# Optimization experiments

Measured on AMD Instinct MI355X. Metric: run time of the kernel, lower is better.

## Reference

```python
import jax, jax.numpy as jnp
import numpy as np

BS, F, C, H, W = 2, 8, 64, 128, 128
HEADS = 4

def build_edges(bs, f):
    rows, cols, ec = [], [], 0
    for b in range(bs):
        s = b * (2 * f + 2)
        v = list(range(s, s + f)); d = list(range(s + f, s + 2 * f))
        t = s + 2 * f; g = t + 1
        for grp in (v, d, v + d, v + d, v + d + [t], [t], [g]):
            rows += grp; cols += [ec] * len(grp); ec += 1
    return np.asarray(rows, np.int32), np.asarray(cols, np.int32), ec

ROW, COL, NUM_EDGES = build_edges(BS, F)

def conv2d_s2(x, w, b):  # Conv2d k3 s2 p1 + ReLU
    y = jax.lax.conv_general_dilated(x, w, (2, 2), [(1, 1), (1, 1)],
        dimension_numbers=('NCHW', 'OIHW', 'NCHW'))
    return jax.nn.relu(y + b[None, :, None, None])

def conv_t2(x, w, b):  # ConvTranspose2d k3 s2 p1 op1 + ReLU; w: (in,out,3,3)
    wt = jnp.flip(w, (2, 3)).transpose(1, 0, 2, 3)
    y = jax.lax.conv_general_dilated(x, wt, (1, 1), [(1, 2), (1, 2)],
        lhs_dilation=(2, 2), dimension_numbers=('NCHW', 'OIHW', 'NCHW'))
    return jax.nn.relu(y + b[None, :, None, None])

def layer_norm(x, eps=1e-5):  # affine params are default ones/zeros
    mu = x.mean(-1, keepdims=True)
    var = ((x - mu) ** 2).mean(-1, keepdims=True)
    return (x - mu) / jnp.sqrt(var + eps)

def group_norm(x, groups=32, eps=1e-5):
    n, c = x.shape
    xg = x.reshape(n, groups, c // groups)
    mu = xg.mean(-1, keepdims=True)
    var = ((xg - mu) ** 2).mean(-1, keepdims=True)
    return ((xg - mu) / jnp.sqrt(var + eps)).reshape(n, c)

def se_layer(x, w1, w2):  # squeeze over node dim 0
    y = jax.nn.sigmoid(jax.nn.relu(x.mean(0) @ w1.T) @ w2.T)
    return x * y

def hypergraph_conv(x, lin_w, att, edge_w, edge_attr, out_ch):
    # PyG HypergraphConv, use_attention=True, attention_mode='node', heads=4,
    # concat=False, bias=False, eval mode (dropout inactive)
    n = x.shape[0]
    xl = (x @ lin_w.T).reshape(n, HEADS, out_ch)
    ea = (edge_attr @ lin_w.T).reshape(-1, HEADS, out_ch)
    a = (jnp.concatenate([xl[ROW], ea[COL]], axis=-1) * att).sum(-1)  # (E, heads)
    a = jax.nn.leaky_relu(a, 0.2)
    a = jnp.exp(a - jax.ops.segment_max(a, COL, num_segments=NUM_EDGES)[COL])
    a = a / (jax.ops.segment_sum(a, COL, num_segments=NUM_EDGES)[COL] + 1e-16)
    D = jax.ops.segment_sum(edge_w[COL], ROW, num_segments=n)
    D = jnp.where(D > 0, 1.0 / D, 0.0)
    B = jax.ops.segment_sum(jnp.ones(ROW.shape[0], x.dtype), COL, num_segments=NUM_EDGES)
    B = jnp.where(B > 0, 1.0 / B, 0.0)
    e = jax.ops.segment_sum(B[COL][:, None, None] * a[:, :, None] * xl[ROW], COL, num_segments=NUM_EDGES)
    o = jax.ops.segment_sum(D[ROW][:, None, None] * a[:, :, None] * e[COL], ROW, num_segments=n)
    return o.mean(1)  # concat=False -> head mean

def setup_inputs() -> dict:
    key = jax.random.key(0)
    ks = jax.random.split(key, 32)
    def n(k, shape, s=1.0):
        return jax.random.normal(k, shape, jnp.float32) * s
    def u(k, shape):
        return jax.random.uniform(k, shape, jnp.float32)
    return {
        'vision_feat': n(ks[0], (BS, F, C, H, W)), 'vision_pos': n(ks[1], (BS, F, C, H, W), 0.1),
        'motion_feat': n(ks[2], (BS, F, C, H, W)), 'motion_pos': n(ks[3], (BS, F, C, H, W), 0.1),
        'text_feat': n(ks[4], (BS, C, 16)), 'text_pos': n(ks[5], (BS, C, 16), 0.1),
        'cv1_w': n(ks[6], (2 * C, C, 3, 3), 0.04), 'cv1_b': n(ks[7], (2 * C,), 0.01),
        'cv2_w': n(ks[8], (4 * C, 2 * C, 3, 3), 0.03), 'cv2_b': n(ks[9], (4 * C,), 0.01),
        'dc1_w': n(ks[10], (2 * C, C, 3, 3), 0.04), 'dc1_b': n(ks[11], (2 * C,), 0.01),
        'dc2_w': n(ks[12], (4 * C, 2 * C, 3, 3), 0.03), 'dc2_b': n(ks[13], (4 * C,), 0.01),
        'tc1_w': n(ks[14], (4 * C, 2 * C, 3, 3), 0.03), 'tc1_b': n(ks[15], (2 * C,), 0.01),
        'tc2_w': n(ks[16], (2 * C, C, 3, 3), 0.04), 'tc2_b': n(ks[17], (C,), 0.01),
        'lin1_w': n(ks[18], (HEADS * 8 * C, 4 * C), 0.06), 'att1': n(ks[19], (1, HEADS, 16 * C), 0.05),
        'lin2_w': n(ks[20], (HEADS * 4 * C, 8 * C), 0.04), 'att2': n(ks[21], (1, HEADS, 8 * C), 0.05),
        'ew1': u(ks[22], (2 * F * BS + 2,)), 'ew2': u(ks[23], (2 * F * BS + 2,)),
        'ea1': u(ks[24], (2 * F * BS + 2, 4 * C)), 'ea2': u(ks[25], (2 * F * BS + 2, 8 * C)),
        'se1_w1': n(ks[26], (8 * C // 16, 8 * C), 0.06), 'se1_w2': n(ks[27], (8 * C, 8 * C // 16), 0.15),
        'se2_w1': n(ks[28], (4 * C // 16, 4 * C), 0.08), 'se2_w2': n(ks[29], (4 * C, 4 * C // 16), 0.2),
    }

def reference(vision_feat, vision_pos, motion_feat, motion_pos, text_feat, text_pos,
              cv1_w, cv1_b, cv2_w, cv2_b, dc1_w, dc1_b, dc2_w, dc2_b,
              tc1_w, tc1_b, tc2_w, tc2_b, lin1_w, att1, lin2_w, att2,
              ew1, ew2, ea1, ea2, se1_w1, se1_w2, se2_w1, se2_w2):
    bs, f, c, h, w = vision_feat.shape
    # text_pool: AdaptiveMaxPool1d(4) on L=16 -> exact windows of 4; view(bs,-1)
    tn = (text_feat + text_pos).reshape(bs, c, 4, 4).max(-1).reshape(bs, 4 * c)
    v0 = (vision_feat + vision_pos).reshape(bs * f, c, h, w)
    v1 = conv2d_s2(v0, cv1_w, cv1_b)          # (bs*f, 2c, h/2, w/2)
    v2 = conv2d_s2(v1, cv2_w, cv2_b)          # (bs*f, 4c, h/4, w/4)
    vn = layer_norm(v2.max((2, 3)))           # AdaptiveMaxPool2d(1) + LayerNorm
    d0 = (motion_feat + motion_pos).reshape(bs * f, c, h, w)
    dn = layer_norm(conv2d_s2(conv2d_s2(d0, dc1_w, dc1_b), dc2_w, dc2_b).max((2, 3)))
    vb = vn.reshape(bs, f, 4 * c); db = dn.reshape(bs, f, 4 * c)
    obs = tn + (vb + db).mean(1)              # observer = mean(text+v+d) over frames
    x = jnp.concatenate([vb, db, tn[:, None], obs[:, None]], axis=1).reshape(bs * (2 * f + 2), 4 * c)
    x = se_layer(group_norm(jax.nn.relu(hypergraph_conv(x, lin1_w, att1, ew1, ea1, 8 * c))), se1_w1, se1_w2)
    x = se_layer(group_norm(jax.nn.relu(hypergraph_conv(x, lin2_w, att2, ew2, ea2, 4 * c))), se2_w1, se2_w2)
    xb = x.reshape(bs, 2 * f + 2, 4 * c)
    # obs_pool: AdaptiveMaxPool1d(c) on L=4c -> windows of 4
    observers = (tn + xb[:, -1]).reshape(bs, c, 4).max(-1)
    vg = xb[:, :f].reshape(bs * f, 4 * c)
    # bilinear upsample of 1x1 == broadcast; transconv doubles size so the
    # subsequent F.interpolate calls to (h/2,w/2) and (h,w) are identities
    vr = v2 + vg[:, :, None, None]
    vr = v1 + conv_t2(vr, tc1_w, tc1_b)
    vr = v0 + conv_t2(vr, tc2_w, tc2_b)
    return vr, observers
```

## Files before the change

### kernel.cpp

```cpp
#include <hip/hip_runtime.h>
#include <hip/hip_bf16.h>
#include <cstddef>
#include <cstdint>

#define DEV_INLINE __device__ __forceinline__

typedef __attribute__((ext_vector_type(8))) short short8;
typedef __attribute__((ext_vector_type(4))) float f32x4;
typedef __attribute__((ext_vector_type(2))) float f32x2;
typedef __attribute__((ext_vector_type(4))) unsigned short us4;

DEV_INLINE unsigned short f2bf(float f) {
  uint32_t u = __builtin_bit_cast(uint32_t, f);
  uint32_t r = (u + 0x7fffu + ((u >> 16) & 1u)) >> 16;
  return (unsigned short)r;
}
DEV_INLINE float bf2f(unsigned short u) {
  return __builtin_bit_cast(float, (uint32_t)u << 16);
}

__device__ __constant__ int c_cs[15] = {0,8,16,32,48,65,66,67,75,83,99,115,132,133,134};
__device__ __constant__ int c_row[134] = {
  0,1,2,3,4,5,6,7,
  8,9,10,11,12,13,14,15,
  0,1,2,3,4,5,6,7,8,9,10,11,12,13,14,15,
  0,1,2,3,4,5,6,7,8,9,10,11,12,13,14,15,
  0,1,2,3,4,5,6,7,8,9,10,11,12,13,14,15,16,
  16,
  17,
  18,19,20,21,22,23,24,25,
  26,27,28,29,30,31,32,33,
  18,19,20,21,22,23,24,25,26,27,28,29,30,31,32,33,
  18,19,20,21,22,23,24,25,26,27,28,29,30,31,32,33,
  18,19,20,21,22,23,24,25,26,27,28,29,30,31,32,33,34,
  34,
  35
};
__device__ __constant__ int c_col[134] = {
  0,0,0,0,0,0,0,0,
  1,1,1,1,1,1,1,1,
  2,2,2,2,2,2,2,2,2,2,2,2,2,2,2,2,
  3,3,3,3,3,3,3,3,3,3,3,3,3,3,3,3,
  4,4,4,4,4,4,4,4,4,4,4,4,4,4,4,4,4,
  5,
  6,
  7,7,7,7,7,7,7,7,
  8,8,8,8,8,8,8,8,
  9,9,9,9,9,9,9,9,9,9,9,9,9,9,9,9,
  10,10,10,10,10,10,10,10,10,10,10,10,10,10,10,10,
  11,11,11,11,11,11,11,11,11,11,11,11,11,11,11,11,11,
  12,
  13
};

__global__ __launch_bounds__(256) void k_prep(const float* __restrict__ a,
                                              const float* __restrict__ b,
                                              unsigned short* __restrict__ o) {
  int bid = blockIdx.x;
  int xb = bid & 1, y = (bid >> 1) & 127, n = bid >> 8;
  __shared__ unsigned int su[32][65];
  int t = threadIdx.x;
  const size_t base = ((size_t)n * 64) * 16384 + (size_t)y * 128 + xb * 64;
  float4 A0[2], B0[2], A1[2], B1[2];
#pragma unroll
  for (int it = 0; it < 2; ++it) {
    int i = t + it * 256;
    int cpair = i >> 4, x4 = i & 15;
    size_t off = base + (size_t)(2 * cpair) * 16384 + x4 * 4;
    A0[it] = *reinterpret_cast<const float4*>(a + off);
    B0[it] = *reinterpret_cast<const float4*>(b + off);
    A1[it] = *reinterpret_cast<const float4*>(a + off + 16384);
    B1[it] = *reinterpret_cast<const float4*>(b + off + 16384);
  }
#pragma unroll
  for (int it = 0; it < 2; ++it) {
    int i = t + it * 256;
    int cpair = i >> 4, x4 = i & 15;
    unsigned int* row = &su[cpair][x4 * 4];
    row[0] = (unsigned int)f2bf(A0[it].x + B0[it].x) | ((unsigned int)f2bf(A1[it].x + B1[it].x) << 16);
    row[1] = (unsigned int)f2bf(A0[it].y + B0[it].y) | ((unsigned int)f2bf(A1[it].y + B1[it].y) << 16);
    row[2] = (unsigned int)f2bf(A0[it].z + B0[it].z) | ((unsigned int)f2bf(A1[it].z + B1[it].z) << 16);
    row[3] = (unsigned int)f2bf(A0[it].w + B0[it].w) | ((unsigned int)f2bf(A1[it].w + B1[it].w) << 16);
  }
  __syncthreads();
  unsigned int* op = (unsigned int*)(o + (((size_t)n * 128 + y) * 128 + xb * 64) * 64);
#pragma unroll
  for (int it = 0; it < 2; ++it) {
    int i = t + it * 256;
    int x = i >> 3, cq = i & 7;
    uint4 v;
    v.x = su[cq * 4 + 0][x];
    v.y = su[cq * 4 + 1][x];
    v.z = su[cq * 4 + 2][x];
    v.w = su[cq * 4 + 3][x];
    *reinterpret_cast<uint4*>(op + x * 32 + cq * 4) = v;
  }
}

__global__ void k_wtrans_all(const float* __restrict__ cv1w, const float* __restrict__ dc1w,
                             const float* __restrict__ cv2w, const float* __restrict__ dc2w,
                             const float* __restrict__ tc1w, const float* __restrict__ tc2w,
                             unsigned short* __restrict__ wtb) {
  int idx = blockIdx.x * 256 + threadIdx.x;
  const float* src; int off, lci, lco; bool tra;
  if (idx < 73728)        { src = cv1w; off = 0;       lci = 6; lco = 7; tra = false; }
  else if (idx < 147456)  { src = dc1w; off = 73728;   lci = 6; lco = 7; tra = false; }
  else if (idx < 442368)  { src = cv2w; off = 147456;  lci = 7; lco = 8; tra = false; }
  else if (idx < 737280)  { src = dc2w; off = 442368;  lci = 7; lco = 8; tra = false; }
  else if (idx < 1032192) { src = tc1w; off = 737280;  lci = 8; lco = 7; tra = true;  }
  else if (idx < 1105920) { src = tc2w; off = 1032192; lci = 7; lco = 6; tra = true;  }
  else return;
  int l = idx - off;
  int ci = l & ((1 << lci) - 1);
  int r = l >> lci;
  int co = r & ((1 << lco) - 1);
  int tap = r >> lco;
  size_t si = tra ? (((size_t)ci << lco) + co) * 9 + tap
                  : (((size_t)co << lci) + ci) * 9 + tap;
  wtb[idx] = f2bf(src[si]);
}

template<int CI, int CO, int HO, int WO, int ROUT>
__global__ __launch_bounds__(512, 3) void k_conv_mfma(
    const unsigned short* __restrict__ in,
    const unsigned short* __restrict__ wT,
    const float* __restrict__ bias,
    unsigned short* __restrict__ outn) {
  constexpr int HIN = HO * 2, WIN = WO * 2;
  constexpr int XHP = WO + 2;
  constexpr int R = 2 * ROUT + 1;
  constexpr int NPOS = R * 2 * XHP;
  constexpr int NCH = NPOS * 4;
  constexpr int NCS = CI / 32;
  constexpr int KIT = (NCH + 511) / 512;
  constexpr int CB = CO / 128;
  constexpr int OB = HO / ROUT;
  __shared__ short8 sIn[NPOS * 5];
  int bid = blockIdx.x;
  int cb = bid % CB; bid /= CB;
  int oyb = bid % OB; int n = bid / OB;
  int tid = threadIdx.x;
  int wid = tid >> 6, lane = tid & 63;
  int wm = wid >> 1, wn = wid & 1;
  int llo = lane & 15, lhi = lane >> 4;
  f32x4 acc[2][2] = {};
  const int iy0 = oyb * (2 * ROUT) - 1;
  short8 rv[KIT];
  auto loadr = [&](int cs) {
#pragma unroll
    for (int k = 0; k < KIT; ++k) {
      int i = tid + k * 512;
      short8 v = {};
      if (i < NCH) {
        int c = i & 3, q = i >> 2;
        int xh = q % XHP; int q2 = q / XHP;
        int p = q2 & 1, l = q2 >> 1;
        int x = 2 * xh + p - 1;
        int iy = iy0 + l;
        if (x >= 0 && x < WIN && iy >= 0 && iy < HIN)
          v = *reinterpret_cast<const short8*>(in + ((((size_t)n * HIN + iy) * WIN + x) * CI + cs * 32 + c * 8));
      }
      rv[k] = v;
    }
  };
  auto writes = [&]() {
#pragma unroll
    for (int k = 0; k < KIT; ++k) {
      int i = tid + k * 512;
      if (i < NCH) sIn[(i >> 2) * 5 + (i & 3)] = rv[k];
    }
  };
  loadr(0);
  for (int cs = 0; cs < NCS; ++cs) {
    writes();
    __syncthreads();
    if (cs + 1 < NCS) loadr(cs + 1);
    short8 afr9[9][2];
#pragma unroll
    for (int tap = 0; tap < 9; ++tap)
#pragma unroll
      for (int m = 0; m < 2; ++m) {
        int co = cb * 128 + wm * 32 + m * 16 + llo;
        afr9[tap][m] = *reinterpret_cast<const short8*>(wT + (((size_t)tap * CO + co) * CI + cs * 32 + lhi * 8));
      }
#pragma unroll
    for (int tap = 0; tap < 9; ++tap) {
      const int ky = tap / 3, kx = tap % 3;
      short8 bfr[2];
#pragma unroll
      for (int n2 = 0; n2 < 2; ++n2) {
        int pix = wn * 32 + n2 * 16 + llo;
        int oyl = (ROUT == 2) ? (pix >> 5) : 0;
        int ox = pix - oyl * WO;
        int lrow = 2 * oyl + ky;
        int pos = (lrow * 2 + (kx & 1)) * XHP + ox + (kx >> 1);
        bfr[n2] = sIn[pos * 5 + lhi];
      }
#pragma unroll
      for (int m = 0; m < 2; ++m)
#pragma unroll
        for (int n2 = 0; n2 < 2; ++n2)
          acc[m][n2] = __builtin_amdgcn_mfma_f32_16x16x32_bf16(afr9[tap][m], bfr[n2], acc[m][n2], 0, 0, 0);
    }
    __syncthreads();
  }
#pragma unroll
  for (int m = 0; m < 2; ++m) {
    int co0 = cb * 128 + wm * 32 + m * 16 + lhi * 4;
    f32x4 bv = *reinterpret_cast<const f32x4*>(bias + co0);
#pragma unroll
    for (int n2 = 0; n2 < 2; ++n2) {
      int pix = wn * 32 + n2 * 16 + llo;
      int oyl = (ROUT == 2) ? (pix >> 5) : 0;
      int ox = pix - oyl * WO;
      int oy = oyb * ROUT + oyl;
      us4 pk;
      pk[0] = f2bf(fmaxf(acc[m][n2][0] + bv[0], 0.f));
      pk[1] = f2bf(fmaxf(acc[m][n2][1] + bv[1], 0.f));
      pk[2] = f2bf(fmaxf(acc[m][n2][2] + bv[2], 0.f));
      pk[3] = f2bf(fmaxf(acc[m][n2][3] + bv[3], 0.f));
      *reinterpret_cast<us4*>(outn + ((((size_t)n * HO + oy) * WO + ox) * CO + co0)) = pk;
    }
  }
}

template<int CI, int CO, int Hi, int Wi, int QR, bool OBF, bool GADD>
__global__ __launch_bounds__(256, 3) void k_deconv_mfma(
    const unsigned short* __restrict__ in,
    const unsigned short* __restrict__ wT,
    const float* __restrict__ bias,
    const unsigned short* __restrict__ resn,
    const float* __restrict__ gsrc,
    unsigned short* __restrict__ outn,
    float* __restrict__ outc) {
  constexpr int QC = 64 / QR;
  constexpr int WP = Wi + 1;
  constexpr int NPOS = (QR + 1) * WP;
  constexpr int NCH = NPOS * 4;
  constexpr int NCS = CI / 32;
  constexpr int KIT = (NCH + 255) / 256;
  constexpr int CB = CO / 64;
  constexpr int OB = Hi / QR;
  constexpr int Ho = Hi * 2, Wo = Wi * 2;
  __shared__ short8 sIn[NPOS * 5];
  int bid = blockIdx.x;
  int cb = bid % CB; bid /= CB;
  int oyb = bid % OB; int n = bid / OB;
  int tid = threadIdx.x;
  int wid = tid >> 6, lane = tid & 63;
  int wm = wid >> 1, wn = wid & 1;
  int llo = lane & 15, lhi = lane >> 4;
  int qy0 = oyb * QR;
  const float* g = nullptr;
  if constexpr (GADD) g = gsrc + ((size_t)((n >> 3) * 18 + (n & 7))) * 256;
  f32x4 acc[4][2][2] = {};
  constexpr int tap_p[9] = {3,2,3,1,0,1,3,2,3};
  constexpr int tap_b[9] = {3,2,2,1,0,0,1,0,0};
  short8 rv[KIT];
  auto loadr = [&](int cs) {
#pragma unroll
    for (int k = 0; k < KIT; ++k) {
      int i = tid + k * 256;
      short8 v = {};
      if (i < NCH) {
        int c = i & 3, q = i >> 2;
        int x = q % WP, l = q / WP;
        int iy = qy0 + l;
        if (x < Wi && iy < Hi) {
          v = *reinterpret_cast<const short8*>(in + (((size_t)(n * Hi + iy) * Wi + x) * CI + cs * 32 + c * 8));
          if constexpr (GADD) {
#pragma unroll
            for (int j = 0; j < 8; ++j) {
              float fv = bf2f((unsigned short)v[j]) + g[cs * 32 + c * 8 + j];
              v[j] = (short)f2bf(fv);
            }
          }
        }
      }
      rv[k] = v;
    }
  };
  auto writes = [&]() {
#pragma unroll
    for (int k = 0; k < KIT; ++k) {
      int i = tid + k * 256;
      if (i < NCH) sIn[(i >> 2) * 5 + (i & 3)] = rv[k];
    }
  };
  loadr(0);
  for (int cs = 0; cs < NCS; ++cs) {
    writes();
    __syncthreads();
    if (cs + 1 < NCS) loadr(cs + 1);
    short8 bfr[2][4];
#pragma unroll
    for (int n2 = 0; n2 < 2; ++n2) {
      int pix = wn * 32 + n2 * 16 + llo;
      int qyl = pix / QC, qx = pix % QC;
#pragma unroll
      for (int bs = 0; bs < 4; ++bs) {
        int pos = (qyl + (bs >> 1)) * WP + qx + (bs & 1);
        bfr[n2][bs] = sIn[pos * 5 + lhi];
      }
    }
#pragma unroll
    for (int m = 0; m < 2; ++m) {
      short8 afr9[9];
#pragma unroll
      for (int tap = 0; tap < 9; ++tap) {
        int co = cb * 64 + wm * 32 + m * 16 + llo;
        afr9[tap] = *reinterpret_cast<const short8*>(wT + (((size_t)tap * CO + co) * CI + cs * 32 + lhi * 8));
      }
#pragma unroll
      for (int tap = 0; tap < 9; ++tap)
#pragma unroll
        for (int n2 = 0; n2 < 2; ++n2)
          acc[tap_p[tap]][m][n2] = __builtin_amdgcn_mfma_f32_16x16x32_bf16(
              afr9[tap], bfr[n2][tap_b[tap]], acc[tap_p[tap]][m][n2], 0, 0, 0);
    }
    __syncthreads();
  }
#pragma unroll
  for (int m = 0; m < 2; ++m) {
    int co0 = cb * 64 + wm * 32 + m * 16 + lhi * 4;
    f32x4 bv = *reinterpret_cast<const f32x4*>(bias + co0);
#pragma unroll
    for (int n2 = 0; n2 < 2; ++n2) {
      int pix = wn * 32 + n2 * 16 + llo;
      int qyl = pix / QC, qx = pix % QC;
      int qy = qy0 + qyl;
      if constexpr (OBF) {
#pragma unroll
        for (int p = 0; p < 4; ++p) {
          int oy = 2 * qy + (p >> 1);
          int ox = 2 * qx + (p & 1);
          size_t ad = ((size_t)(n * Ho + oy) * Wo + ox) * CO + co0;
          us4 r = *reinterpret_cast<const us4*>(resn + ad);
          us4 pk;
#pragma unroll
          for (int c = 0; c < 4; ++c)
            pk[c] = f2bf(bf2f(r[c]) + fmaxf(acc[p][m][n2][c] + bv[c], 0.f));
          *reinterpret_cast<us4*>(outn + ad) = pk;
        }
      } else {
        int qx2 = 2 * qx;
#pragma unroll
        for (int dy = 0; dy < 2; ++dy) {
          int oy = 2 * qy + dy;
          size_t rb = ((size_t)(n * Ho + oy) * Wo + qx2) * CO + co0;
          us4 r0 = *reinterpret_cast<const us4*>(resn + rb);
          us4 r1 = *reinterpret_cast<const us4*>(resn + rb + CO);
#pragma unroll
          for (int c = 0; c < 4; ++c) {
            f32x2 st;
            st[0] = bf2f(r0[c]) + fmaxf(acc[dy * 2][m][n2][c] + bv[c], 0.f);
            st[1] = bf2f(r1[c]) + fmaxf(acc[dy * 2 + 1][m][n2][c] + bv[c], 0.f);
            __builtin_nontemporal_store(st,
                reinterpret_cast<f32x2*>(outc + ((size_t)(n * CO + co0 + c) * Ho + oy) * Wo + qx2));
          }
        }
      }
    }
  }
}

__global__ __launch_bounds__(256) void k_max_part(const unsigned short* __restrict__ x,
                                                  float* __restrict__ pmax) {
  int n = blockIdx.x >> 3, pg = blockIdx.x & 7;
  int t = threadIdx.x;
  int c8 = t & 31;
  int ps = t >> 5;
  const unsigned short* base = x + (size_t)n * 262144 + (size_t)pg * 32768 + (size_t)c8 * 8;
  float m[8];
#pragma unroll
  for (int j = 0; j < 8; ++j) m[j] = -1e30f;
  for (int p = ps * 16; p < ps * 16 + 16; ++p) {
    short8 v = *reinterpret_cast<const short8*>(base + (size_t)p * 256);
#pragma unroll
    for (int j = 0; j < 8; ++j) m[j] = fmaxf(m[j], bf2f((unsigned short)v[j]));
  }
  __shared__ float sred[8][264];
#pragma unroll
  for (int j = 0; j < 8; ++j) sred[ps][c8 * 8 + j] = m[j];
  __syncthreads();
  float mm = sred[0][t];
#pragma unroll
  for (int g = 1; g < 8; ++g) mm = fmaxf(mm, sred[g][t]);
  pmax[((size_t)n * 8 + pg) * 256 + t] = mm;
}

__global__ __launch_bounds__(256) void k_ln(const float* __restrict__ pmax,
                                            float* __restrict__ out) {
  int n = blockIdx.x, ch = threadIdx.x;
  float m = -1e30f;
#pragma unroll
  for (int g = 0; g < 8; ++g)
    m = fmaxf(m, pmax[((size_t)n * 8 + g) * 256 + ch]);
  __shared__ float r1[256], r2[256];
  r1[ch] = m; __syncthreads();
  for (int s = 128; s > 0; s >>= 1) { if (ch < s) r1[ch] += r1[ch + s]; __syncthreads(); }
  float mu = r1[0] * (1.f / 256.f);
  float d = m - mu;
  r2[ch] = d * d; __syncthreads();
  for (int s = 128; s > 0; s >>= 1) { if (ch < s) r2[ch] += r2[ch + s]; __syncthreads(); }
  out[(size_t)n * 256 + ch] = d * rsqrtf(r2[0] * (1.f / 256.f) + 1e-5f);
}

__global__ void k_build_x(const float* __restrict__ tf, const float* __restrict__ tp,
                          const float* __restrict__ vn, const float* __restrict__ dn,
                          float* __restrict__ tn, float* __restrict__ x0) {
  int b = blockIdx.x, ch = threadIdx.x;
  int c4 = ch >> 2, j = ch & 3;
  const float* p = tf + ((size_t)b * 64 + c4) * 16 + j * 4;
  const float* q = tp + ((size_t)b * 64 + c4) * 16 + j * 4;
  float tv = p[0] + q[0];
  tv = fmaxf(tv, p[1] + q[1]);
  tv = fmaxf(tv, p[2] + q[2]);
  tv = fmaxf(tv, p[3] + q[3]);
  tn[(size_t)b * 256 + ch] = tv;
  float s = 0.f;
  for (int f = 0; f < 8; ++f) {
    float vv = vn[((size_t)b * 8 + f) * 256 + ch];
    float dd = dn[((size_t)b * 8 + f) * 256 + ch];
    s += vv + dd;
    x0[((size_t)b * 18 + f) * 256 + ch] = vv;
    x0[((size_t)b * 18 + 8 + f) * 256 + ch] = dd;
  }
  x0[((size_t)b * 18 + 16) * 256 + ch] = tv;
  x0[((size_t)b * 18 + 17) * 256 + ch] = tv + s * (1.f / 8.f);
}

__global__ __launch_bounds__(256) void k_gnn_lin(
    const float* __restrict__ x, const float* __restrict__ ea,
    const float* __restrict__ w, float* __restrict__ y, int K, int M) {
  int chunks = M >> 8;
  int r = blockIdx.x / chunks;
  int ob = (blockIdx.x % chunks) * 256 + threadIdx.x;
  const float* src = (r < 36) ? (x + (size_t)r * K) : (ea + (size_t)(r - 36) * K);
  __shared__ __align__(16) float sxr[512];
  for (int k = threadIdx.x; k < K; k += 256) sxr[k] = src[k];
  __syncthreads();
  const float4* w4 = reinterpret_cast<const float4*>(w + (size_t)ob * K);
  const float4* x4 = reinterpret_cast<const float4*>(sxr);
  float acc = 0.f;
  int k4 = K >> 2;
  for (int k = 0; k < k4; ++k) {
    float4 a = x4[k], b = w4[k];
    acc += a.x * b.x + a.y * b.y + a.z * b.z + a.w * b.w;
  }
  y[(size_t)r * M + ob] = acc;
}

template<int OC>
__global__ __launch_bounds__(256) void k_gnn_attsm(
    const float* __restrict__ y, const float* __restrict__ att,
    float* __restrict__ attw) {
  int t = threadIdx.x;
  __shared__ float sx_s[144], seb_s[60];
  __shared__ float a_s[536];
  if (t < 200) {
    int r = t >> 2, h = t & 3;
    const float4* row = reinterpret_cast<const float4*>(y + ((size_t)r * 4 + h) * OC);
    const float4* ar = reinterpret_cast<const float4*>(att + (size_t)h * 2 * OC + (r < 36 ? 0 : OC));
    float s = 0.f;
#pragma unroll 4
    for (int k = 0; k < OC / 4; ++k) {
      float4 a = row[k], b = ar[k];
      s += a.x * b.x + a.y * b.y + a.z * b.z + a.w * b.w;
    }
    if (r < 36) sx_s[r * 4 + h] = s; else seb_s[(r - 36) * 4 + h] = s;
  }
  __syncthreads();
  for (int idx = t; idx < 536; idx += 256) {
    int i = idx >> 2, h = idx & 3;
    float v = sx_s[c_row[i] * 4 + h] + seb_s[c_col[i] * 4 + h];
    a_s[idx] = (v > 0.f) ? v : 0.2f * v;
  }
  __syncthreads();
  if (t < 56) {
    int c = t >> 2, h = t & 3;
    int st = c_cs[c], en = c_cs[c + 1];
    float m = -1e30f;
    for (int i = st; i < en; ++i) m = fmaxf(m, a_s[i * 4 + h]);
    float s = 0.f;
    for (int i = st; i < en; ++i) { float e = __expf(a_s[i * 4 + h] - m); a_s[i * 4 + h] = e; s += e; }
    float inv = 1.f / (s + 1e-16f);
    for (int i = st; i < en; ++i) a_s[i * 4 + h] *= inv;
  }
  __syncthreads();
  for (int idx = t; idx < 536; idx += 256) attw[idx] = a_s[idx];
}

template<int OC>
__global__ __launch_bounds__(256) void k_edge_agg(
    const float* __restrict__ y, const float* __restrict__ attw,
    float* __restrict__ eb) {
  int idx = blockIdx.x * 256 + threadIdx.x;
  if (idx >= 14 * 4 * OC) return;
  int ch = idx % OC;
  int h = (idx / OC) & 3;
  int c = idx / (4 * OC);
  int st = c_cs[c], en = c_cs[c + 1];
  float s = 0.f;
  for (int i = st; i < en; ++i)
    s += attw[i * 4 + h] * y[(size_t)c_row[i] * (4 * OC) + h * OC + ch];
  eb[idx] = s * (1.f / (float)(en - st));
}

template<int OC>
__global__ __launch_bounds__(256) void k_node_agg(
    const float* __restrict__ attw, const float* __restrict__ eb,
    const float* __restrict__ ew, float* __restrict__ ho) {
  int idx = blockIdx.x * 256 + threadIdx.x;
  if (idx >= 36 * OC) return;
  int ch = idx % OC;
  int node = idx / OC;
  int b = node / 18, ln = node % 18;
  int ncols, cols[4], gis[4];
  if (ln < 16) {
    ncols = 4;
    cols[0] = b * 7 + (ln < 8 ? 0 : 1); gis[0] = b * 67 + ln;
    cols[1] = b * 7 + 2; gis[1] = b * 67 + 16 + ln;
    cols[2] = b * 7 + 3; gis[2] = b * 67 + 32 + ln;
    cols[3] = b * 7 + 4; gis[3] = b * 67 + 48 + ln;
  } else if (ln == 16) {
    ncols = 2;
    cols[0] = b * 7 + 4; gis[0] = b * 67 + 64;
    cols[1] = b * 7 + 5; gis[1] = b * 67 + 65;
    cols[2] = cols[3] = 0; gis[2] = gis[3] = 0;
  } else {
    ncols = 1;
    cols[0] = b * 7 + 6; gis[0] = b * 67 + 66;
    cols[1] = cols[2] = cols[3] = 0; gis[1] = gis[2] = gis[3] = 0;
  }
  float dsum = 0.f;
#pragma unroll
  for (int k = 0; k < 4; ++k) if (k < ncols) dsum += ew[cols[k]];
  float D = dsum > 0.f ? 1.f / dsum : 0.f;
  float s = 0.f;
#pragma unroll
  for (int k = 0; k < 4; ++k) {
    if (k < ncols) {
#pragma unroll
      for (int h = 0; h < 4; ++h)
        s += attw[gis[k] * 4 + h] * eb[((size_t)cols[k] * 4 + h) * OC + ch];
    }
  }
  ho[idx] = fmaxf(0.25f * D * s, 0.f);
}

template<int C, int Cr>
__global__ __launch_bounds__(512) void k_gn_se(
    const float* __restrict__ hin, const float* __restrict__ w1,
    const float* __restrict__ w2, float* __restrict__ x) {
  int t = threadIdx.x;
  constexpr int gs = C >> 5;
  for (int idx = t; idx < 36 * 32; idx += 512) {
    int node = idx >> 5, g = idx & 31;
    const float* p = hin + (size_t)node * C + g * gs;
    float s = 0.f, s2 = 0.f;
#pragma unroll
    for (int k = 0; k < gs; ++k) { float v = p[k]; s += v; s2 += v * v; }
    float mu = s * (1.f / gs);
    float var = s2 * (1.f / gs) - mu * mu;
    float inv = rsqrtf(fmaxf(var, 0.f) + 1e-5f);
    float* q = x + (size_t)node * C + g * gs;
#pragma unroll
    for (int k = 0; k < gs; ++k) q[k] = (p[k] - mu) * inv;
  }
  __threadfence_block();
  __syncthreads();
  __shared__ float smean[C];
  __shared__ float spart[Cr][17];
  __shared__ float shid[Cr];
  __shared__ float sscale[C];
  if (t < C) {
    float s = 0.f;
    for (int nn = 0; nn < 36; ++nn) s += x[(size_t)nn * C + t];
    smean[t] = s * (1.f / 36.f);
  }
  __syncthreads();
  if (t < Cr * 16) {
    int hid = t >> 4, sub = t & 15;
    constexpr int CH = C / 16;
    float s = 0.f;
#pragma unroll
    for (int k = 0; k < CH; ++k)
      s += w1[(size_t)hid * C + sub * CH + k] * smean[sub * CH + k];
    spart[hid][sub] = s;
  }
  __syncthreads();
  if (t < Cr) {
    float s = 0.f;
#pragma unroll
    for (int k = 0; k < 16; ++k) s += spart[t][k];
    shid[t] = fmaxf(s, 0.f);
  }
  __syncthreads();
  if (t < C) {
    float s = 0.f;
#pragma unroll
    for (int k = 0; k < Cr; ++k) s += w2[(size_t)t * Cr + k] * shid[k];
    sscale[t] = 1.f / (1.f + __expf(-s));
  }
  __syncthreads();
  for (int idx = t; idx < 36 * C; idx += 512) x[idx] *= sscale[idx % C];
}

__global__ void k_obs(const float* __restrict__ tn, const float* __restrict__ x2,
                      float* __restrict__ out) {
  int t = threadIdx.x;
  if (t >= 128) return;
  int b = t >> 6, ch = t & 63;
  const float* a = tn + (size_t)b * 256 + ch * 4;
  const float* c = x2 + ((size_t)b * 18 + 17) * 256 + ch * 4;
  float m = a[0] + c[0];
  m = fmaxf(m, a[1] + c[1]);
  m = fmaxf(m, a[2] + c[2]);
  m = fmaxf(m, a[3] + c[3]);
  out[b * 64 + ch] = m;
}

extern "C" void kernel_launch(void* const* d_in, const int* in_sizes, int n_in,
                              void* d_out, int out_size, void* d_ws, size_t ws_size,
                              hipStream_t stream) {
  (void)in_sizes; (void)n_in; (void)out_size; (void)ws_size;
  const float* vf    = (const float*)d_in[0];
  const float* vp    = (const float*)d_in[1];
  const float* mf    = (const float*)d_in[2];
  const float* mp    = (const float*)d_in[3];
  const float* tf    = (const float*)d_in[4];
  const float* tp    = (const float*)d_in[5];
  const float* cv1w  = (const float*)d_in[6];
  const float* cv1b  = (const float*)d_in[7];
  const float* cv2w  = (const float*)d_in[8];
  const float* cv2b  = (const float*)d_in[9];
  const float* dc1w  = (const float*)d_in[10];
  const float* dc1b  = (const float*)d_in[11];
  const float* dc2w  = (const float*)d_in[12];
  const float* dc2b  = (const float*)d_in[13];
  const float* tc1w  = (const float*)d_in[14];
  const float* tc1b  = (const float*)d_in[15];
  const float* tc2w  = (const float*)d_in[16];
  const float* tc2b  = (const float*)d_in[17];
  const float* lin1w = (const float*)d_in[18];
  const float* att1  = (const float*)d_in[19];
  const float* lin2w = (const float*)d_in[20];
  const float* att2  = (const float*)d_in[21];
  const float* ew1   = (const float*)d_in[22];
  const float* ew2   = (const float*)d_in[23];
  const float* ea1   = (const float*)d_in[24];
  const float* ea2   = (const float*)d_in[25];
  const float* se1w1 = (const float*)d_in[26];
  const float* se1w2 = (const float*)d_in[27];
  const float* se2w1 = (const float*)d_in[28];
  const float* se2w2 = (const float*)d_in[29];

  float* ws  = (float*)d_ws;
  float* out = (float*)d_out;

  unsigned short* p0n = (unsigned short*)(ws);
  unsigned short* q1n = (unsigned short*)(ws + 8388608);
  unsigned short* t1n = (unsigned short*)(ws + 12582912);
  unsigned short* v2n = (unsigned short*)(ws + 16777216);
  unsigned short* wtb = (unsigned short*)(ws + 18874368);
  float* sm   = ws + 19427328;
  float* tn   = sm;
  float* vn   = sm + 512;
  float* dn   = sm + 4608;
  float* x0   = sm + 8704;
  float* xl   = sm + 17920;
  float* eb   = sm + 120520;
  float* ho   = sm + 149192;
  float* x1   = sm + 167624;
  float* x2   = sm + 186056;
  float* attw = sm + 195272;
  float* pmax = sm + 195904;

  unsigned short* wTc1 = wtb;
  unsigned short* wTd1 = wtb + 73728;
  unsigned short* wTc2 = wtb + 147456;
  unsigned short* wTd2 = wtb + 442368;
  unsigned short* wTt1 = wtb + 737280;
  unsigned short* wTt2 = wtb + 1032192;

  k_wtrans_all<<<4320, 256, 0, stream>>>(cv1w, dc1w, cv2w, dc2w, tc1w, tc2w, wtb);

  k_prep<<<4096, 256, 0, stream>>>(mf, mp, p0n);
  k_conv_mfma<64, 128, 64, 64, 1><<<1024, 512, 0, stream>>>(p0n, wTd1, dc1b, q1n);
  k_conv_mfma<128, 256, 32, 32, 2><<<512, 512, 0, stream>>>(q1n, wTd2, dc2b, v2n);
  k_max_part<<<128, 256, 0, stream>>>(v2n, pmax);
  k_ln<<<16, 256, 0, stream>>>(pmax, dn);

  k_prep<<<4096, 256, 0, stream>>>(vf, vp, p0n);
  k_conv_mfma<64, 128, 64, 64, 1><<<1024, 512, 0, stream>>>(p0n, wTc1, cv1b, q1n);
  k_conv_mfma<128, 256, 32, 32, 2><<<512, 512, 0, stream>>>(q1n, wTc2, cv2b, v2n);
  k_max_part<<<128, 256, 0, stream>>>(v2n, pmax);
  k_ln<<<16, 256, 0, stream>>>(pmax, vn);

  k_build_x<<<2, 256, 0, stream>>>(tf, tp, vn, dn, tn, x0);

  k_gnn_lin<<<50 * 8, 256, 0, stream>>>(x0, ea1, lin1w, xl, 256, 2048);
  k_gnn_attsm<512><<<1, 256, 0, stream>>>(xl, att1, attw);
  k_edge_agg<512><<<112, 256, 0, stream>>>(xl, attw, eb);
  k_node_agg<512><<<72, 256, 0, stream>>>(attw, eb, ew1, ho);
  k_gn_se<512, 32><<<1, 512, 0, stream>>>(ho, se1w1, se1w2, x1);

  k_gnn_lin<<<50 * 4, 256, 0, stream>>>(x1, ea2, lin2w, xl, 512, 1024);
  k_gnn_attsm<256><<<1, 256, 0, stream>>>(xl, att2, attw);
  k_edge_agg<256><<<56, 256, 0, stream>>>(xl, attw, eb);
  k_node_agg<256><<<36, 256, 0, stream>>>(attw, eb, ew2, ho);
  k_gn_se<256, 16><<<1, 512, 0, stream>>>(ho, se2w1, se2w2, x2);

  k_obs<<<1, 128, 0, stream>>>(tn, x2, out + 16777216);

  k_deconv_mfma<256, 128, 32, 32, 2, true, true><<<512, 256, 0, stream>>>(
      v2n, wTt1, tc1b, q1n, x2, t1n, nullptr);
  k_deconv_mfma<128, 64, 64, 64, 1, false, false><<<1024, 256, 0, stream>>>(
      t1n, wTt2, tc2b, p0n, nullptr, nullptr, out);
}
```

Measured before the change: 482.7 us.

## Halve deconv pixel tile per block and load prep inputs directly into LDS

The transposed-conv kernel now tiles along x as well (QW columns), so each block covers 32 quad-pixels instead of 64. That doubles the grid, halves the accumulator registers and raises the occupancy target to 4. The cost is weight fragments fetched from global once per tap for half as many pixels, plus a larger halo overhead. The prep kernel now uses global_load_lds to stage the fp32 a/b tiles directly into shared memory and does the add and bf16 pack on the read side, avoiding register staging.

```diff
diff --git a/kernel.cpp b/kernel.cpp
--- a/kernel.cpp
+++ b/kernel.cpp
@@ -4,6 +4,8 @@
 #include <cstdint>
 
 #define DEV_INLINE __device__ __forceinline__
+#define AS1 __attribute__((address_space(1)))
+#define AS3 __attribute__((address_space(3)))
 
 typedef __attribute__((ext_vector_type(8))) short short8;
 typedef __attribute__((ext_vector_type(4))) float f32x4;
@@ -17,6 +19,11 @@
 }
 DEV_INLINE float bf2f(unsigned short u) {
   return __builtin_bit_cast(float, (uint32_t)u << 16);
+}
+
+DEV_INLINE void gl_lds16(const float* g, float* l) {
+  __builtin_amdgcn_global_load_lds((AS1 void*)const_cast<float*>(g),
+                                   (AS3 void*)l, 16, 0, 0);
 }
 
 __device__ __constant__ int c_cs[15] = {0,8,16,32,48,65,66,67,75,83,99,115,132,133,134};
@@ -56,43 +63,42 @@
 __global__ __launch_bounds__(256) void k_prep(const float* __restrict__ a,
                                               const float* __restrict__ b,
                                               unsigned short* __restrict__ o) {
+  __shared__ float sa[16 * 260];
+  __shared__ float sb[16 * 260];
   int bid = blockIdx.x;
   int xb = bid & 1, y = (bid >> 1) & 127, n = bid >> 8;
-  __shared__ unsigned int su[32][65];
   int t = threadIdx.x;
+  int w = t >> 6, lane = t & 63;
+  int ciq = lane >> 4;
+  int xo = (lane & 15) * 4;
   const size_t base = ((size_t)n * 64) * 16384 + (size_t)y * 128 + xb * 64;
-  float4 A0[2], B0[2], A1[2], B1[2];
-#pragma unroll
-  for (int it = 0; it < 2; ++it) {
-    int i = t + it * 256;
-    int cpair = i >> 4, x4 = i & 15;
-    size_t off = base + (size_t)(2 * cpair) * 16384 + x4 * 4;
-    A0[it] = *reinterpret_cast<const float4*>(a + off);
-    B0[it] = *reinterpret_cast<const float4*>(b + off);
-    A1[it] = *reinterpret_cast<const float4*>(a + off + 16384);
-    B1[it] = *reinterpret_cast<const float4*>(b + off + 16384);
-  }
-#pragma unroll
-  for (int it = 0; it < 2; ++it) {
-    int i = t + it * 256;
-    int cpair = i >> 4, x4 = i & 15;
-    unsigned int* row = &su[cpair][x4 * 4];
-    row[0] = (unsigned int)f2bf(A0[it].x + B0[it].x) | ((unsigned int)f2bf(A1[it].x + B1[it].x) << 16);
-    row[1] = (unsigned int)f2bf(A0[it].y + B0[it].y) | ((unsigned int)f2bf(A1[it].y + B1[it].y) << 16);
-    row[2] = (unsigned int)f2bf(A0[it].z + B0[it].z) | ((unsigned int)f2bf(A1[it].z + B1[it].z) << 16);
-    row[3] = (unsigned int)f2bf(A0[it].w + B0[it].w) | ((unsigned int)f2bf(A1[it].w + B1[it].w) << 16);
-  }
-  __syncthreads();
+#pragma unroll
+  for (int k = 0; k < 4; ++k) {
+    int row = w * 16 + k * 4;
+    const float* ga = a + base + (size_t)(row + ciq) * 16384 + xo;
+    const float* gb = b + base + (size_t)(row + ciq) * 16384 + xo;
+    gl_lds16(ga, &sa[(4 * w + k) * 260]);
+    gl_lds16(gb, &sb[(4 * w + k) * 260]);
+  }
+  __syncthreads();
+  auto rd = [](const float* s, int ci, int x) {
+    return s[(ci >> 2) * 260 + (ci & 3) * 64 + x];
+  };
   unsigned int* op = (unsigned int*)(o + (((size_t)n * 128 + y) * 128 + xb * 64) * 64);
 #pragma unroll
   for (int it = 0; it < 2; ++it) {
     int i = t + it * 256;
     int x = i >> 3, cq = i & 7;
     uint4 v;
-    v.x = su[cq * 4 + 0][x];
-    v.y = su[cq * 4 + 1][x];
-    v.z = su[cq * 4 + 2][x];
-    v.w = su[cq * 4 + 3][x];
+    unsigned int vv[4];
+#pragma unroll
+    for (int j = 0; j < 4; ++j) {
+      int c2 = cq * 8 + j * 2;
+      unsigned int lo = f2bf(rd(sa, c2, x) + rd(sb, c2, x));
+      unsigned int hi = f2bf(rd(sa, c2 + 1, x) + rd(sb, c2 + 1, x));
+      vv[j] = lo | (hi << 16);
+    }
+    v.x = vv[0]; v.y = vv[1]; v.z = vv[2]; v.w = vv[3];
     *reinterpret_cast<uint4*>(op + x * 32 + cq * 4) = v;
   }
 }
@@ -224,8 +230,8 @@
   }
 }
 
-template<int CI, int CO, int Hi, int Wi, int QR, bool OBF, bool GADD>
-__global__ __launch_bounds__(256, 3) void k_deconv_mfma(
+template<int CI, int CO, int Hi, int Wi, int QR, int QW, bool OBF, bool GADD>
+__global__ __launch_bounds__(256, 4) void k_deconv_mfma(
     const unsigned short* __restrict__ in,
     const unsigned short* __restrict__ wT,
     const float* __restrict__ bias,
@@ -233,27 +239,30 @@
     const float* __restrict__ gsrc,
     unsigned short* __restrict__ outn,
     float* __restrict__ outc) {
-  constexpr int QC = 64 / QR;
-  constexpr int WP = Wi + 1;
+  constexpr int WP = QW + 1;
   constexpr int NPOS = (QR + 1) * WP;
   constexpr int NCH = NPOS * 4;
   constexpr int NCS = CI / 32;
   constexpr int KIT = (NCH + 255) / 256;
   constexpr int CB = CO / 64;
+  constexpr int XS = Wi / QW;
   constexpr int OB = Hi / QR;
   constexpr int Ho = Hi * 2, Wo = Wi * 2;
   __shared__ short8 sIn[NPOS * 5];
   int bid = blockIdx.x;
   int cb = bid % CB; bid /= CB;
+  int xs = bid % XS; bid /= XS;
   int oyb = bid % OB; int n = bid / OB;
   int tid = threadIdx.x;
   int wid = tid >> 6, lane = tid & 63;
   int wm = wid >> 1, wn = wid & 1;
   int llo = lane & 15, lhi = lane >> 4;
-  int qy0 = oyb * QR;
+  int qy0 = oyb * QR, qx0 = xs * QW;
+  int pix = wn * 16 + llo;
+  int qyl = pix / QW, qxl = pix % QW;
   const float* g = nullptr;
   if constexpr (GADD) g = gsrc + ((size_t)((n >> 3) * 18 + (n & 7))) * 256;
-  f32x4 acc[4][2][2] = {};
+  f32x4 acc[4][2] = {};
   constexpr int tap_p[9] = {3,2,3,1,0,1,3,2,3};
   constexpr int tap_b[9] = {3,2,2,1,0,0,1,0,0};
   short8 rv[KIT];
@@ -264,7 +273,8 @@
       short8 v = {};
       if (i < NCH) {
         int c = i & 3, q = i >> 2;
-        int x = q % WP, l = q / WP;
+        int xl = q % WP, l = q / WP;
+        int x = qx0 + xl;
         int iy = qy0 + l;
         if (x < Wi && iy < Hi) {
           v = *reinterpret_cast<const short8*>(in + (((size_t)(n * Hi + iy) * Wi + x) * CI + cs * 32 + c * 8));
@@ -292,31 +302,24 @@
     writes();
     __syncthreads();
     if (cs + 1 < NCS) loadr(cs + 1);
-    short8 bfr[2][4];
-#pragma unroll
-    for (int n2 = 0; n2 < 2; ++n2) {
-      int pix = wn * 32 + n2 * 16 + llo;
-      int qyl = pix / QC, qx = pix % QC;
-#pragma unroll
-      for (int bs = 0; bs < 4; ++bs) {
-        int pos = (qyl + (bs >> 1)) * WP + qx + (bs & 1);
-        bfr[n2][bs] = sIn[pos * 5 + lhi];
+    short8 bfr[4];
+#pragma unroll
+    for (int bs = 0; bs < 4; ++bs) {
+      int pos = (qyl + (bs >> 1)) * WP + qxl + (bs & 1);
+      bfr[bs] = sIn[pos * 5 + lhi];
+    }
+#pragma unroll
+    for (int tap = 0; tap < 9; ++tap) {
+      short8 afr[2];
+#pragma unroll
+      for (int m = 0; m < 2; ++m) {
+        int co = cb * 64 + wm * 32 + m * 16 + llo;
+        afr[m] = *reinterpret_cast<const short8*>(wT + (((size_t)tap * CO + co) * CI + cs * 32 + lhi * 8));
       }
-    }
-#pragma unroll
-    for (int m = 0; m < 2; ++m) {
-      short8 afr9[9];
-#pragma unroll
-      for (int tap = 0; tap < 9; ++tap) {
-        int co = cb * 64 + wm * 32 + m * 16 + llo;
-        afr9[tap] = *reinterpret_cast<const short8*>(wT + (((size_t)tap * CO + co) * CI + cs * 32 + lhi * 8));
-      }
-#pragma unroll
-      for (int tap = 0; tap < 9; ++tap)
-#pragma unroll
-        for (int n2 = 0; n2 < 2; ++n2)
-          acc[tap_p[tap]][m][n2] = __builtin_amdgcn_mfma_f32_16x16x32_bf16(
-              afr9[tap], bfr[n2][tap_b[tap]], acc[tap_p[tap]][m][n2], 0, 0, 0);
+#pragma unroll
+      for (int m = 0; m < 2; ++m)
+        acc[tap_p[tap]][m] = __builtin_amdgcn_mfma_f32_16x16x32_bf16(
+            afr[m], bfr[tap_b[tap]], acc[tap_p[tap]][m], 0, 0, 0);
     }
     __syncthreads();
   }
@@ -324,40 +327,35 @@
   for (int m = 0; m < 2; ++m) {
     int co0 = cb * 64 + wm * 32 + m * 16 + lhi * 4;
     f32x4 bv = *reinterpret_cast<const f32x4*>(bias + co0);
-#pragma unroll
-    for (int n2 = 0; n2 < 2; ++n2) {
-      int pix = wn * 32 + n2 * 16 + llo;
-      int qyl = pix / QC, qx = pix % QC;
-      int qy = qy0 + qyl;
-      if constexpr (OBF) {
-#pragma unroll
-        for (int p = 0; p < 4; ++p) {
-          int oy = 2 * qy + (p >> 1);
-          int ox = 2 * qx + (p & 1);
-          size_t ad = ((size_t)(n * Ho + oy) * Wo + ox) * CO + co0;
-          us4 r = *reinterpret_cast<const us4*>(resn + ad);
-          us4 pk;
-#pragma unroll
-          for (int c = 0; c < 4; ++c)
-            pk[c] = f2bf(bf2f(r[c]) + fmaxf(acc[p][m][n2][c] + bv[c], 0.f));
-          *reinterpret_cast<us4*>(outn + ad) = pk;
-        }
-      } else {
-        int qx2 = 2 * qx;
-#pragma unroll
-        for (int dy = 0; dy < 2; ++dy) {
-          int oy = 2 * qy + dy;
-          size_t rb = ((size_t)(n * Ho + oy) * Wo + qx2) * CO + co0;
-          us4 r0 = *reinterpret_cast<const us4*>(resn + rb);
-          us4 r1 = *reinterpret_cast<const us4*>(resn + rb + CO);
-#pragma unroll
-          for (int c = 0; c < 4; ++c) {
-            f32x2 st;
-            st[0] = bf2f(r0[c]) + fmaxf(acc[dy * 2][m][n2][c] + bv[c], 0.f);
-            st[1] = bf2f(r1[c]) + fmaxf(acc[dy * 2 + 1][m][n2][c] + bv[c], 0.f);
-            __builtin_nontemporal_store(st,
-                reinterpret_cast<f32x2*>(outc + ((size_t)(n * CO + co0 + c) * Ho + oy) * Wo + qx2));
-          }
+    int qy = qy0 + qyl, qx = qx0 + qxl;
+    if constexpr (OBF) {
+#pragma unroll
+      for (int p = 0; p < 4; ++p) {
+        int oy = 2 * qy + (p >> 1);
+        int ox = 2 * qx + (p & 1);
+        size_t ad = ((size_t)(n * Ho + oy) * Wo + ox) * CO + co0;
+        us4 r = *reinterpret_cast<const us4*>(resn + ad);
+        us4 pk;
+#pragma unroll
+        for (int c = 0; c < 4; ++c)
+          pk[c] = f2bf(bf2f(r[c]) + fmaxf(acc[p][m][c] + bv[c], 0.f));
+        *reinterpret_cast<us4*>(outn + ad) = pk;
+      }
+    } else {
+      int qx2 = 2 * qx;
+#pragma unroll
+      for (int dy = 0; dy < 2; ++dy) {
+        int oy = 2 * qy + dy;
+        size_t rb = ((size_t)(n * Ho + oy) * Wo + qx2) * CO + co0;
+        us4 r0 = *reinterpret_cast<const us4*>(resn + rb);
+        us4 r1 = *reinterpret_cast<const us4*>(resn + rb + CO);
+#pragma unroll
+        for (int c = 0; c < 4; ++c) {
+          f32x2 st;
+          st[0] = bf2f(r0[c]) + fmaxf(acc[dy * 2][m][c] + bv[c], 0.f);
+          st[1] = bf2f(r1[c]) + fmaxf(acc[dy * 2 + 1][m][c] + bv[c], 0.f);
+          __builtin_nontemporal_store(st,
+              reinterpret_cast<f32x2*>(outc + ((size_t)(n * CO + co0 + c) * Ho + oy) * Wo + qx2));
         }
       }
     }
@@ -714,8 +712,8 @@
 
   k_obs<<<1, 128, 0, stream>>>(tn, x2, out + 16777216);
 
-  k_deconv_mfma<256, 128, 32, 32, 2, true, true><<<512, 256, 0, stream>>>(
+  k_deconv_mfma<256, 128, 32, 32, 2, 16, true, true><<<1024, 256, 0, stream>>>(
       v2n, wTt1, tc1b, q1n, x2, t1n, nullptr);
-  k_deconv_mfma<128, 64, 64, 64, 1, false, false><<<1024, 256, 0, stream>>>(
+  k_deconv_mfma<128, 64, 64, 64, 1, 32, false, false><<<2048, 256, 0, stream>>>(
       t1n, wTt2, tc2b, p0n, nullptr, nullptr, out);
 }
```

New measurement: 534.8 us. 10.8% more time.
